# Kernel tuning notes

Measured on AMD Instinct MI355X. Metric: run time of the kernel, lower is better.

## Reference

```python
import jax, jax.numpy as jnp
import numpy as np

HIDDEN = 1024
NUM_HEADS = 16
HEAD_DIM = HIDDEN // NUM_HEADS


def rotary_cos_sin(seq_len, head_dim, dtype=jnp.float32):
    inv_freq = 1.0 / (10000.0 ** (jnp.arange(0, head_dim, 2, dtype=dtype) / head_dim))
    t = jnp.arange(seq_len, dtype=dtype)
    freqs = jnp.einsum('i,j->ij', t, inv_freq)          # [S, hd/2]
    emb = jnp.concatenate([freqs, freqs], axis=-1)      # [S, hd]
    return jnp.cos(emb), jnp.sin(emb)


def apply_rotary(x, cos, sin):
    # x: [B, H, S, hd]; cos/sin: [S, hd]
    x1, x2 = jnp.split(x, 2, axis=-1)
    x_rot = jnp.concatenate([-x2, x1], axis=-1)
    return x * cos + x_rot * sin


def setup_inputs() -> dict:
    key = jax.random.key(0)
    ks = jax.random.split(key, 5)
    S, B = 2048, 2
    x = jax.random.normal(ks[0], (S, B, HIDDEN), dtype=jnp.float32)
    s = 1.0 / np.sqrt(HIDDEN)
    W_qkv = jax.random.uniform(ks[1], (HIDDEN, 3 * HIDDEN), jnp.float32, -s, s)
    b_qkv = jax.random.uniform(ks[2], (3 * HIDDEN,), jnp.float32, -s, s)
    W_out = jax.random.uniform(ks[3], (HIDDEN, HIDDEN), jnp.float32, -s, s)
    b_out = jax.random.uniform(ks[4], (HIDDEN,), jnp.float32, -s, s)
    return {"x": x, "W_qkv": W_qkv, "b_qkv": b_qkv, "W_out": W_out, "b_out": b_out}


def reference(x, W_qkv, b_qkv, W_out, b_out):
    S, B, D = x.shape
    scale = HEAD_DIM ** -0.5
    qkv = x @ W_qkv + b_qkv                               # [S, B, 3D]
    qkv = qkv.reshape(S, B, NUM_HEADS, 3 * HEAD_DIM)
    q, k, v = jnp.split(qkv, 3, axis=-1)                  # each [S, B, H, hd]
    q = q.transpose(1, 2, 0, 3)                           # [B, H, S, hd]
    k = k.transpose(1, 2, 0, 3)
    v = v.transpose(1, 2, 0, 3)
    cos, sin = rotary_cos_sin(S, HEAD_DIM, x.dtype)
    q = apply_rotary(q, cos, sin)
    k = apply_rotary(k, cos, sin)
    scores = jnp.einsum('bhqd,bhkd->bhqk', q, k) * scale  # [B, H, S, S]
    weights = jax.nn.softmax(scores, axis=-1)
    attn = jnp.einsum('bhqk,bhkd->bhqd', weights, v)      # [B, H, S, hd]
    attn = attn.transpose(2, 0, 1, 3).reshape(S, B, D)    # [S, B, D]
    return attn @ W_out + b_out
```

## Files before the change

### kernel.cpp

```cpp
#include <hip/hip_runtime.h>

typedef unsigned short u16;
typedef __attribute__((ext_vector_type(8))) short bf16x8;
typedef __attribute__((ext_vector_type(4))) float f32x4;

#define S_LEN 2048
#define BATCH 2
#define HID 1024
#define NH 16
#define HD 64
#define MROWS 4096
#define QKV_N 3072
#define QSCALE 0.18033688011112042f

__device__ __forceinline__ u16 f2bf(float f) {
  unsigned u = __float_as_uint(f);
  u += 0x7fffu + ((u >> 16) & 1u);
  return (u16)(u >> 16);
}

__device__ __forceinline__ float bf2f(u16 u) {
  return __uint_as_float((unsigned)u << 16);
}

__device__ __forceinline__ float fexp2(float x) {
  float r; asm("v_exp_f32 %0, %1" : "=v"(r) : "v"(x)); return r;
}

__device__ __forceinline__ unsigned cvtpk(float lo, float hi) {
  unsigned r; asm("v_cvt_pk_bf16_f32 %0, %1, %2" : "=v"(r) : "v"(lo), "v"(hi)); return r;
}

__device__ __forceinline__ void gl2lds16(const u16* src, u16* lds) {
  __builtin_amdgcn_global_load_lds((__attribute__((address_space(1))) void*)(void*)src,
                                   (__attribute__((address_space(3))) void*)(void*)lds,
                                   16, 0, 0);
}

__device__ __forceinline__ void castT_body(const float* __restrict__ W, u16* __restrict__ Wt,
                                           int Ncols, int Krows, int bx, int by,
                                           float (*tile)[33]) {
  int c0 = bx * 32, r0 = by * 32;
  int tx = threadIdx.x & 31, ty = threadIdx.x >> 5;
  #pragma unroll
  for (int i = 0; i < 4; ++i)
    tile[ty + i * 8][tx] = W[(size_t)(r0 + ty + i * 8) * Ncols + c0 + tx];
  __syncthreads();
  #pragma unroll
  for (int i = 0; i < 4; ++i) {
    int a = ty + i * 8;
    Wt[(size_t)(c0 + a) * Krows + r0 + tx] = f2bf(tile[tx][a]);
  }
}

__global__ __launch_bounds__(256) void prep(
    const float* __restrict__ x, const float* __restrict__ W_qkv,
    const float* __restrict__ W_out, u16* __restrict__ xb,
    u16* __restrict__ Wqt, u16* __restrict__ Wot, float2* __restrict__ rope) {
  __shared__ float tile[32][33];
  const int bid = blockIdx.x;
  if (bid < 2048) {
    int i = bid * 256 + threadIdx.x;
    const float4* p = (const float4*)x;
    float4 a = p[2 * i], b = p[2 * i + 1];
    union { u16 us[8]; uint4 v; } o;
    o.us[0] = f2bf(a.x); o.us[1] = f2bf(a.y); o.us[2] = f2bf(a.z); o.us[3] = f2bf(a.w);
    o.us[4] = f2bf(b.x); o.us[5] = f2bf(b.y); o.us[6] = f2bf(b.z); o.us[7] = f2bf(b.w);
    *(uint4*)&xb[8 * i] = o.v;
  } else if (bid < 2048 + 3072) {
    int r = bid - 2048;
    castT_body(W_qkv, Wqt, QKV_N, HID, r % 96, r / 96, tile);
  } else if (bid < 2048 + 3072 + 1024) {
    int r = bid - (2048 + 3072);
    castT_body(W_out, Wot, HID, HID, r % 32, r / 32, tile);
  } else {
    int i = (bid - 6144) * 256 + threadIdx.x;
    int s = i >> 5, j = i & 31;
    float invf = powf(10000.0f, -(float)(2 * j) / 64.0f);
    float ang = (float)s * invf;
    rope[i] = make_float2(cosf(ang), sinf(ang));
  }
}

__global__ __launch_bounds__(256, 2) void gemm_qkv(
    const u16* __restrict__ A, const u16* __restrict__ Bt,
    const float* __restrict__ bias, const float2* __restrict__ rope,
    u16* __restrict__ Qb, u16* __restrict__ Kb, u16* __restrict__ Vb) {
  __shared__ u16 As[128 * 32];
  __shared__ u16 Bs[128 * 32];
  const int tid = threadIdx.x;
  const int lane = tid & 63, wid = tid >> 6;
  const int g = lane >> 4, l15 = lane & 15;
  const int bm0 = blockIdx.x * 128, bn0 = blockIdx.y * 128;
  const int wm = wid >> 1, wn = wid & 1;

  f32x4 acc[4][4] = {};
  for (int kt = 0; kt < 32; ++kt) {
    const int k0 = kt * 32;
    __syncthreads();
    #pragma unroll
    for (int it = 0; it < 2; ++it) {
      int s = it * 256 + tid;
      gl2lds16(A  + (size_t)(bm0 + (s >> 2)) * 1024 + k0 + (s & 3) * 8, &As[s * 8]);
      gl2lds16(Bt + (size_t)(bn0 + (s >> 2)) * 1024 + k0 + (s & 3) * 8, &Bs[s * 8]);
    }
    __syncthreads();
    bf16x8 af[4], bfr[4];
    #pragma unroll
    for (int m = 0; m < 4; ++m) af[m]  = *(const bf16x8*)&As[(wm * 64 + m * 16 + l15) * 32 + g * 8];
    #pragma unroll
    for (int n = 0; n < 4; ++n) bfr[n] = *(const bf16x8*)&Bs[(wn * 64 + n * 16 + l15) * 32 + g * 8];
    #pragma unroll
    for (int m = 0; m < 4; ++m)
      #pragma unroll
      for (int n = 0; n < 4; ++n)
        acc[m][n] = __builtin_amdgcn_mfma_f32_16x16x32_bf16(af[m], bfr[n], acc[m][n], 0, 0, 0);
  }

  const int cw0 = bn0 + wn * 64;
  const int gi = cw0 >> 6;
  const int h = gi / 3, tt = gi % 3;
  float bs[4];
  #pragma unroll
  for (int n = 0; n < 4; ++n) bs[n] = bias[cw0 + n * 16 + l15];
  const size_t hb = (size_t)h * (S_LEN * HD);

  if (tt == 2) {
    #pragma unroll
    for (int m = 0; m < 4; ++m)
      #pragma unroll
      for (int reg = 0; reg < 4; ++reg) {
        int r = bm0 + wm * 64 + m * 16 + g * 4 + reg;
        int srow = r >> 1, b = r & 1;
        size_t o = (size_t)(b * NH) * (S_LEN * HD) + hb + (size_t)srow * HD;
        #pragma unroll
        for (int n = 0; n < 4; ++n)
          Vb[o + n * 16 + l15] = f2bf(acc[m][n][reg] + bs[n]);
      }
  } else {
    u16* dst = (tt == 0) ? Qb : Kb;
    const float scl = (tt == 0) ? QSCALE : 1.0f;
    #pragma unroll
    for (int m = 0; m < 4; ++m)
      #pragma unroll
      for (int reg = 0; reg < 4; ++reg) {
        int r = bm0 + wm * 64 + m * 16 + g * 4 + reg;
        int srow = r >> 1, b = r & 1;
        size_t o = (size_t)(b * NH) * (S_LEN * HD) + hb + (size_t)srow * HD;
        #pragma unroll
        for (int n = 0; n < 2; ++n) {
          int dlo = n * 16 + l15;
          float2 cs = rope[srow * 32 + dlo];
          float v1 = acc[m][n][reg] + bs[n];
          float v2 = acc[m][n + 2][reg] + bs[n + 2];
          dst[o + dlo]      = f2bf((v1 * cs.x - v2 * cs.y) * scl);
          dst[o + dlo + 32] = f2bf((v2 * cs.x + v1 * cs.y) * scl);
        }
      }
  }
}

__global__ __launch_bounds__(256) void transpose_v(const u16* __restrict__ Vb, u16* __restrict__ Vt) {
  __shared__ u16 t[64][72];
  const int bh = blockIdx.y, s0 = blockIdx.x * 64;
  const size_t base = (size_t)bh * S_LEN * HD;
  const int tid = threadIdx.x;
  #pragma unroll
  for (int it = 0; it < 2; ++it) {
    int sl = it * 256 + tid;
    int r = sl >> 3, cg = sl & 7;
    union { uint4 v; u16 us[8]; } u;
    u.v = *(const uint4*)&Vb[base + (size_t)(s0 + r) * HD + cg * 8];
    #pragma unroll
    for (int j = 0; j < 8; ++j) t[cg * 8 + j][r] = u.us[j];
  }
  __syncthreads();
  #pragma unroll
  for (int it = 0; it < 2; ++it) {
    int sl = it * 256 + tid;
    int d = sl >> 3, sg = sl & 7;
    union { uint4 v; u16 us[8]; } u;
    #pragma unroll
    for (int j = 0; j < 8; ++j) u.us[j] = t[d][sg * 8 + j];
    *(uint4*)&Vt[(size_t)bh * HD * S_LEN + (size_t)d * S_LEN + s0 + sg * 8] = u.v;
  }
}

__global__ __launch_bounds__(512, 8) void attn_fwd(
    const u16* __restrict__ Qb, const u16* __restrict__ Kb,
    const u16* __restrict__ Vt, u16* __restrict__ part0,
    u16* __restrict__ part1, float2* __restrict__ stats) {
  __shared__ u16 Ks[2][64 * 64];
  __shared__ u16 Vs[2][64 * 64];
  const int tid = threadIdx.x;
  const int lane = tid & 63, wid = tid >> 6;
  const int g = lane >> 4, l15 = lane & 15;
  const int bh = blockIdx.y;
  const int split = blockIdx.z;
  const int kt0 = split * 16;
  const int qr0 = blockIdx.x * 128 + wid * 16;
  const u16* Qp = Qb + ((size_t)bh * S_LEN + qr0) * HD;
  const u16* Kp = Kb + (size_t)bh * S_LEN * HD;
  const u16* Vp = Vt + (size_t)bh * HD * S_LEN;

  const int sr = tid >> 3;
  const int ssw = (tid & 7) ^ (sr & 7);
  const u16* kg = Kp + (size_t)sr * HD + ssw * 8;
  const u16* vg = Vp + (size_t)sr * S_LEN + ssw * 8;

  bf16x8 qf[2];
  #pragma unroll
  for (int c = 0; c < 2; ++c) qf[c] = *(const bf16x8*)&Qp[l15 * HD + g * 8 + c * 32];

  f32x4 po[4] = {};
  float mrun = -INFINITY, lrun = 0.f;

  gl2lds16(kg + (size_t)kt0 * 64 * HD, &Ks[0][tid * 8]);
  gl2lds16(vg + kt0 * 64, &Vs[0][tid * 8]);
  __syncthreads();

  for (int i = 0; i < 16; ++i) {
    const int bb = i & 1;
    if (i + 1 < 16) {
      gl2lds16(kg + (size_t)(kt0 + i + 1) * 64 * HD, &Ks[bb ^ 1][tid * 8]);
      gl2lds16(vg + (kt0 + i + 1) * 64, &Vs[bb ^ 1][tid * 8]);
    }
    const u16* KsB = Ks[bb];
    const u16* VsB = Vs[bb];

    f32x4 sacc[4] = {};
    __builtin_amdgcn_s_setprio(1);
    #pragma unroll
    for (int c = 0; c < 2; ++c) {
      const int csw = ((g + 4 * c) ^ (l15 & 7)) * 8;
      #pragma unroll
      for (int t = 0; t < 4; ++t) {
        const bf16x8 kf = *(const bf16x8*)&KsB[(t * 16 + l15) * 64 + csw];
        sacc[t] = __builtin_amdgcn_mfma_f32_16x16x32_bf16(kf, qf[c], sacc[t], 0, 0, 0);
      }
    }
    __builtin_amdgcn_s_setprio(0);

    float m0 = fmaxf(fmaxf(sacc[0][0], sacc[0][1]), sacc[0][2]);
    float m1 = fmaxf(fmaxf(sacc[0][3], sacc[1][0]), sacc[1][1]);
    float m2 = fmaxf(fmaxf(sacc[1][2], sacc[1][3]), sacc[2][0]);
    float m3 = fmaxf(fmaxf(sacc[2][1], sacc[2][2]), sacc[2][3]);
    float m4 = fmaxf(fmaxf(sacc[3][0], sacc[3][1]), sacc[3][2]);
    float tm = fmaxf(fmaxf(fmaxf(m0, m1), fmaxf(m2, m3)), fmaxf(m4, sacc[3][3]));
    tm = fmaxf(tm, __shfl_xor(tm, 16));
    tm = fmaxf(tm, __shfl_xor(tm, 32));

    if (!__all(tm <= mrun + 8.f)) {
      float mnew = fmaxf(mrun, tm);
      float alpha = fexp2(mrun - mnew);
      mrun = mnew;
      lrun *= alpha;
      float ar[4];
      #pragma unroll
      for (int reg = 0; reg < 4; ++reg) ar[reg] = __shfl(alpha, g * 4 + reg);
      #pragma unroll
      for (int n = 0; n < 4; ++n)
        #pragma unroll
        for (int reg = 0; reg < 4; ++reg) po[n][reg] *= ar[reg];
    }

    unsigned u00, u01, u10, u11, u20, u21, u30, u31;
    float rsA, rsB;
    {
      float p0 = fexp2(sacc[0][0] - mrun), p1 = fexp2(sacc[0][1] - mrun);
      float p2 = fexp2(sacc[0][2] - mrun), p3 = fexp2(sacc[0][3] - mrun);
      u00 = cvtpk(p0, p1); u01 = cvtpk(p2, p3);
      rsA = (p0 + p1) + (p2 + p3);
      p0 = fexp2(sacc[1][0] - mrun); p1 = fexp2(sacc[1][1] - mrun);
      p2 = fexp2(sacc[1][2] - mrun); p3 = fexp2(sacc[1][3] - mrun);
      u10 = cvtpk(p0, p1); u11 = cvtpk(p2, p3);
      rsA += (p0 + p1) + (p2 + p3);
      p0 = fexp2(sacc[2][0] - mrun); p1 = fexp2(sacc[2][1] - mrun);
      p2 = fexp2(sacc[2][2] - mrun); p3 = fexp2(sacc[2][3] - mrun);
      u20 = cvtpk(p0, p1); u21 = cvtpk(p2, p3);
      rsB = (p0 + p1) + (p2 + p3);
      p0 = fexp2(sacc[3][0] - mrun); p1 = fexp2(sacc[3][1] - mrun);
      p2 = fexp2(sacc[3][2] - mrun); p3 = fexp2(sacc[3][3] - mrun);
      u30 = cvtpk(p0, p1); u31 = cvtpk(p2, p3);
      rsB += (p0 + p1) + (p2 + p3);
    }
    float rs = rsA + rsB;
    rs += __shfl_xor(rs, 16);
    rs += __shfl_xor(rs, 32);
    lrun += rs;

    asm("v_permlane32_swap_b32 %0, %1" : "+v"(u00), "+v"(u10));
    asm("v_permlane32_swap_b32 %0, %1" : "+v"(u01), "+v"(u11));
    asm("v_permlane32_swap_b32 %0, %1" : "+v"(u20), "+v"(u30));
    asm("v_permlane32_swap_b32 %0, %1" : "+v"(u21), "+v"(u31));
    asm("v_permlane16_swap_b32 %0, %1" : "+v"(u00), "+v"(u10));
    asm("v_permlane16_swap_b32 %0, %1" : "+v"(u01), "+v"(u11));
    asm("v_permlane16_swap_b32 %0, %1" : "+v"(u20), "+v"(u31 == u31 ? u30 : u30));
    asm("v_permlane16_swap_b32 %0, %1" : "+v"(u21), "+v"(u31));
    union { unsigned w[4]; bf16x8 v; } af0, af1;
    af0.w[0] = u00; af0.w[1] = u01; af0.w[2] = u10; af0.w[3] = u11;
    af1.w[0] = u20; af1.w[1] = u21; af1.w[2] = u30; af1.w[3] = u31;

    __builtin_amdgcn_s_setprio(1);
    #pragma unroll
    for (int c = 0; c < 2; ++c) {
      const bf16x8 pf = c ? af1.v : af0.v;
      const int csw = ((g + 4 * c) ^ (l15 & 7)) * 8;
      #pragma unroll
      for (int n = 0; n < 4; ++n) {
        const bf16x8 vf = *(const bf16x8*)&VsB[(n * 16 + l15) * 64 + csw];
        po[n] = __builtin_amdgcn_mfma_f32_16x16x32_bf16(pf, vf, po[n], 0, 0, 0);
      }
    }
    __builtin_amdgcn_s_setprio(0);
    __syncthreads();
  }

  u16* part = split ? part1 : part0;
  if (g == 0)
    stats[(size_t)split * (32 * 2048) + (size_t)bh * 2048 + qr0 + l15] =
        make_float2(mrun, lrun);
  #pragma unroll
  for (int n = 0; n < 4; ++n)
    #pragma unroll
    for (int reg = 0; reg < 4; ++reg) {
      size_t q = (size_t)bh * 2048 + qr0 + g * 4 + reg;
      part[q * 64 + n * 16 + l15] = f2bf(po[n][reg]);
    }
}

__global__ void attn_combine(const u16* __restrict__ part0, const u16* __restrict__ part1,
                             const float2* __restrict__ stats, u16* __restrict__ attn2d) {
  int t = blockIdx.x * 256 + threadIdx.x;
  int bh = t >> 14, r = t & 16383, q = r >> 3, dc = r & 7;
  int b = bh >> 4, h = bh & 15;
  float2 s0 = stats[bh * 2048 + q];
  float2 s1 = stats[32 * 2048 + bh * 2048 + q];
  float M = fmaxf(s0.x, s1.x);
  float w0 = fexp2(s0.x - M), w1 = fexp2(s1.x - M);
  float inv = 1.f / (w0 * s0.y + w1 * s1.y);
  w0 *= inv; w1 *= inv;
  size_t off = ((size_t)bh * 2048 + q) * 64 + dc * 8;
  union { uint4 v; u16 us[8]; } a, c, o;
  a.v = *(const uint4*)&part0[off];
  c.v = *(const uint4*)&part1[off];
  #pragma unroll
  for (int j = 0; j < 8; ++j)
    o.us[j] = f2bf(w0 * bf2f(a.us[j]) + w1 * bf2f(c.us[j]));
  *(uint4*)&attn2d[((size_t)q * BATCH + b) * HID + h * HD + dc * 8] = o.v;
}

__global__ __launch_bounds__(256, 2) void gemm_out(
    const u16* __restrict__ A, const u16* __restrict__ Bt,
    const float* __restrict__ bias, float* __restrict__ out) {
  __shared__ u16 As[128 * 32];
  __shared__ u16 Bs[64 * 32];
  const int tid = threadIdx.x;
  const int lane = tid & 63, wid = tid >> 6;
  const int g = lane >> 4, l15 = lane & 15;
  const int bm0 = blockIdx.x * 128, bn0 = blockIdx.y * 64;

  f32x4 acc[2][4] = {};
  for (int kt = 0; kt < 32; ++kt) {
    const int k0 = kt * 32;
    __syncthreads();
    #pragma unroll
    for (int it = 0; it < 2; ++it) {
      int s = it * 256 + tid;
      gl2lds16(A + (size_t)(bm0 + (s >> 2)) * 1024 + k0 + (s & 3) * 8, &As[s * 8]);
    }
    gl2lds16(Bt + (size_t)(bn0 + (tid >> 2)) * 1024 + k0 + (tid & 3) * 8, &Bs[tid * 8]);
    __syncthreads();
    bf16x8 af[2], bfr[4];
    #pragma unroll
    for (int m = 0; m < 2; ++m) af[m]  = *(const bf16x8*)&As[(wid * 32 + m * 16 + l15) * 32 + g * 8];
    #pragma unroll
    for (int n = 0; n < 4; ++n) bfr[n] = *(const bf16x8*)&Bs[(n * 16 + l15) * 32 + g * 8];
    #pragma unroll
    for (int m = 0; m < 2; ++m)
      #pragma unroll
      for (int n = 0; n < 4; ++n)
        acc[m][n] = __builtin_amdgcn_mfma_f32_16x16x32_bf16(af[m], bfr[n], acc[m][n], 0, 0, 0);
  }
  #pragma unroll
  for (int n = 0; n < 4; ++n) {
    int c = bn0 + n * 16 + l15;
    float bv = bias[c];
    #pragma unroll
    for (int m = 0; m < 2; ++m)
      #pragma unroll
      for (int reg = 0; reg < 4; ++reg) {
        int r = bm0 + wid * 32 + m * 16 + g * 4 + reg;
        out[(size_t)r * HID + c] = acc[m][n][reg] + bv;
      }
  }
}

extern "C" void kernel_launch(void* const* d_in, const int* in_sizes, int n_in,
                              void* d_out, int out_size, void* d_ws, size_t ws_size,
                              hipStream_t stream) {
  const float* x     = (const float*)d_in[0];
  const float* W_qkv = (const float*)d_in[1];
  const float* b_qkv = (const float*)d_in[2];
  const float* W_out = (const float*)d_in[3];
  const float* b_out = (const float*)d_in[4];
  float* out = (float*)d_out;

  char* ws = (char*)d_ws;
  size_t off = 0;
  auto carve = [&](size_t bytes) { void* p = ws + off; off += (bytes + 255) & ~(size_t)255; return p; };
  u16* xb      = (u16*)carve((size_t)MROWS * HID * 2);
  u16* Wqt     = (u16*)carve((size_t)QKV_N * HID * 2);
  u16* Wot     = (u16*)carve((size_t)HID * HID * 2);
  float2* rope = (float2*)carve((size_t)S_LEN * 32 * 8);
  u16* Qb      = (u16*)carve((size_t)BATCH * NH * S_LEN * HD * 2);
  u16* Kb      = (u16*)carve((size_t)BATCH * NH * S_LEN * HD * 2);
  u16* Vb      = (u16*)carve((size_t)BATCH * NH * S_LEN * HD * 2);
  u16* Vt      = (u16*)carve((size_t)BATCH * NH * S_LEN * HD * 2);
  u16* attn2d  = (u16*)carve((size_t)MROWS * HID * 2);
  float2* stats= (float2*)carve((size_t)2 * 32 * 2048 * 8);

  prep<<<6400, 256, 0, stream>>>(x, W_qkv, W_out, xb, Wqt, Wot, rope);
  gemm_qkv<<<dim3(MROWS / 128, QKV_N / 128), 256, 0, stream>>>(xb, Wqt, b_qkv, rope, Qb, Kb, Vb);
  transpose_v<<<dim3(S_LEN / 64, BATCH * NH), 256, 0, stream>>>(Vb, Vt);
  attn_fwd<<<dim3(S_LEN / 128, BATCH * NH, 2), 512, 0, stream>>>(Qb, Kb, Vt, xb, Vb, stats);
  attn_combine<<<2048, 256, 0, stream>>>(xb, Vb, stats, attn2d);
  gemm_out<<<dim3(MROWS / 128, HID / 64), 256, 0, stream>>>(attn2d, Wot, b_out, out);
}
```

Before: 132.6 us.

## Switch attention to 32x32x16 MFMA tiles with 32 query rows per wave

Rewrites the attention forward kernel to use 32x32x16 bf16 MFMA instructions, so each wave handles 32 query rows instead of 16. This halves the number of blocks, and the K rows are permuted at load time so the P fragments line up with the MFMA input layout without permlane swaps. It also remaps the grid to 1D so the two splits of the same head are adjacent, lowers the occupancy hint, and replaces powf with exp2 in the rope table. The larger accumulators raise register pressure, and the halved block count may leave the GPU under-occupied.

```diff
diff --git a/kernel.cpp b/kernel.cpp
--- a/kernel.cpp
+++ b/kernel.cpp
@@ -3,6 +3,7 @@
 typedef unsigned short u16;
 typedef __attribute__((ext_vector_type(8))) short bf16x8;
 typedef __attribute__((ext_vector_type(4))) float f32x4;
+typedef __attribute__((ext_vector_type(16))) float f32x16;
 
 #define S_LEN 2048
 #define BATCH 2
@@ -76,7 +77,7 @@
   } else {
     int i = (bid - 6144) * 256 + threadIdx.x;
     int s = i >> 5, j = i & 31;
-    float invf = powf(10000.0f, -(float)(2 * j) / 64.0f);
+    float invf = fexp2(-(float)(2 * j) * (13.287712379549449f / 64.0f));
     float ang = (float)s * invf;
     rope[i] = make_float2(cosf(ang), sinf(ang));
   }
@@ -186,7 +187,7 @@
   }
 }
 
-__global__ __launch_bounds__(512, 8) void attn_fwd(
+__global__ __launch_bounds__(512, 4) void attn_fwd(
     const u16* __restrict__ Qb, const u16* __restrict__ Kb,
     const u16* __restrict__ Vt, u16* __restrict__ part0,
     u16* __restrict__ part1, float2* __restrict__ stats) {
@@ -194,25 +195,28 @@
   __shared__ u16 Vs[2][64 * 64];
   const int tid = threadIdx.x;
   const int lane = tid & 63, wid = tid >> 6;
-  const int g = lane >> 4, l15 = lane & 15;
-  const int bh = blockIdx.y;
-  const int split = blockIdx.z;
+  const int l31 = lane & 31, h = lane >> 5;
+  const int pp = blockIdx.x & 63;
+  const int bh = pp >> 1, split = pp & 1;
   const int kt0 = split * 16;
-  const int qr0 = blockIdx.x * 128 + wid * 16;
-  const u16* Qp = Qb + ((size_t)bh * S_LEN + qr0) * HD;
+  const int qw0 = (blockIdx.x >> 6) * 256 + wid * 32;
+  const u16* Qp = Qb + ((size_t)bh * S_LEN + qw0) * HD;
   const u16* Kp = Kb + (size_t)bh * S_LEN * HD;
   const u16* Vp = Vt + (size_t)bh * HD * S_LEN;
 
-  const int sr = tid >> 3;
-  const int ssw = (tid & 7) ^ (sr & 7);
-  const u16* kg = Kp + (size_t)sr * HD + ssw * 8;
+  const int sr = tid >> 3, tc = tid & 7;
+  const int ssw = tc ^ (sr & 7);
+  const int act = ((sr >> 4) & 1) * 16 + ((sr >> 2) & 1) * 8
+                + ((sr & 3) | (((sr >> 3) & 1) << 2)) + (sr >> 5) * 32;
+  const u16* kg = Kp + (size_t)act * HD + ssw * 8;
   const u16* vg = Vp + (size_t)sr * S_LEN + ssw * 8;
 
-  bf16x8 qf[2];
-  #pragma unroll
-  for (int c = 0; c < 2; ++c) qf[c] = *(const bf16x8*)&Qp[l15 * HD + g * 8 + c * 32];
-
-  f32x4 po[4] = {};
+  bf16x8 qf0 = *(const bf16x8*)&Qp[(size_t)l31 * HD +  0 + h * 8];
+  bf16x8 qf1 = *(const bf16x8*)&Qp[(size_t)l31 * HD + 16 + h * 8];
+  bf16x8 qf2 = *(const bf16x8*)&Qp[(size_t)l31 * HD + 32 + h * 8];
+  bf16x8 qf3 = *(const bf16x8*)&Qp[(size_t)l31 * HD + 48 + h * 8];
+
+  f32x16 po0 = {}, po1 = {};
   float mrun = -INFINITY, lrun = 0.f;
 
   gl2lds16(kg + (size_t)kt0 * 64 * HD, &Ks[0][tid * 8]);
@@ -228,26 +232,22 @@
     const u16* KsB = Ks[bb];
     const u16* VsB = Vs[bb];
 
-    f32x4 sacc[4] = {};
+    f32x16 s0 = {}, s1 = {};
     __builtin_amdgcn_s_setprio(1);
     #pragma unroll
-    for (int c = 0; c < 2; ++c) {
-      const int csw = ((g + 4 * c) ^ (l15 & 7)) * 8;
-      #pragma unroll
-      for (int t = 0; t < 4; ++t) {
-        const bf16x8 kf = *(const bf16x8*)&KsB[(t * 16 + l15) * 64 + csw];
-        sacc[t] = __builtin_amdgcn_mfma_f32_16x16x32_bf16(kf, qf[c], sacc[t], 0, 0, 0);
-      }
+    for (int s = 0; s < 4; ++s) {
+      const bf16x8 qf = (s == 0) ? qf0 : (s == 1) ? qf1 : (s == 2) ? qf2 : qf3;
+      const int csw = ((2 * s + h) ^ (l31 & 7)) * 8;
+      bf16x8 kf0 = *(const bf16x8*)&KsB[l31 * 64 + csw];
+      s0 = __builtin_amdgcn_mfma_f32_32x32x16_bf16(kf0, qf, s0, 0, 0, 0);
+      bf16x8 kf1 = *(const bf16x8*)&KsB[(32 + l31) * 64 + csw];
+      s1 = __builtin_amdgcn_mfma_f32_32x32x16_bf16(kf1, qf, s1, 0, 0, 0);
     }
     __builtin_amdgcn_s_setprio(0);
 
-    float m0 = fmaxf(fmaxf(sacc[0][0], sacc[0][1]), sacc[0][2]);
-    float m1 = fmaxf(fmaxf(sacc[0][3], sacc[1][0]), sacc[1][1]);
-    float m2 = fmaxf(fmaxf(sacc[1][2], sacc[1][3]), sacc[2][0]);
-    float m3 = fmaxf(fmaxf(sacc[2][1], sacc[2][2]), sacc[2][3]);
-    float m4 = fmaxf(fmaxf(sacc[3][0], sacc[3][1]), sacc[3][2]);
-    float tm = fmaxf(fmaxf(fmaxf(m0, m1), fmaxf(m2, m3)), fmaxf(m4, sacc[3][3]));
-    tm = fmaxf(tm, __shfl_xor(tm, 16));
+    float tm = -INFINITY;
+    #pragma unroll
+    for (int r = 0; r < 16; ++r) tm = fmaxf(tm, fmaxf(s0[r], s1[r]));
     tm = fmaxf(tm, __shfl_xor(tm, 32));
 
     if (!__all(tm <= mrun + 8.f)) {
@@ -255,78 +255,60 @@
       float alpha = fexp2(mrun - mnew);
       mrun = mnew;
       lrun *= alpha;
-      float ar[4];
-      #pragma unroll
-      for (int reg = 0; reg < 4; ++reg) ar[reg] = __shfl(alpha, g * 4 + reg);
-      #pragma unroll
-      for (int n = 0; n < 4; ++n)
-        #pragma unroll
-        for (int reg = 0; reg < 4; ++reg) po[n][reg] *= ar[reg];
-    }
-
-    unsigned u00, u01, u10, u11, u20, u21, u30, u31;
-    float rsA, rsB;
-    {
-      float p0 = fexp2(sacc[0][0] - mrun), p1 = fexp2(sacc[0][1] - mrun);
-      float p2 = fexp2(sacc[0][2] - mrun), p3 = fexp2(sacc[0][3] - mrun);
-      u00 = cvtpk(p0, p1); u01 = cvtpk(p2, p3);
-      rsA = (p0 + p1) + (p2 + p3);
-      p0 = fexp2(sacc[1][0] - mrun); p1 = fexp2(sacc[1][1] - mrun);
-      p2 = fexp2(sacc[1][2] - mrun); p3 = fexp2(sacc[1][3] - mrun);
-      u10 = cvtpk(p0, p1); u11 = cvtpk(p2, p3);
-      rsA += (p0 + p1) + (p2 + p3);
-      p0 = fexp2(sacc[2][0] - mrun); p1 = fexp2(sacc[2][1] - mrun);
-      p2 = fexp2(sacc[2][2] - mrun); p3 = fexp2(sacc[2][3] - mrun);
-      u20 = cvtpk(p0, p1); u21 = cvtpk(p2, p3);
-      rsB = (p0 + p1) + (p2 + p3);
-      p0 = fexp2(sacc[3][0] - mrun); p1 = fexp2(sacc[3][1] - mrun);
-      p2 = fexp2(sacc[3][2] - mrun); p3 = fexp2(sacc[3][3] - mrun);
-      u30 = cvtpk(p0, p1); u31 = cvtpk(p2, p3);
-      rsB += (p0 + p1) + (p2 + p3);
-    }
-    float rs = rsA + rsB;
-    rs += __shfl_xor(rs, 16);
+      #pragma unroll
+      for (int r = 0; r < 16; ++r) {
+        float ar = __shfl(alpha, (r & 3) + 8 * (r >> 2) + 4 * h);
+        po0[r] *= ar;
+        po1[r] *= ar;
+      }
+    }
+
+    float rs = 0.f;
+    unsigned pwa[8], pwb[8];
+    #pragma unroll
+    for (int w = 0; w < 8; ++w) {
+      float a = fexp2(s0[2 * w] - mrun), b = fexp2(s0[2 * w + 1] - mrun);
+      rs += a + b;
+      pwa[w] = cvtpk(a, b);
+    }
+    #pragma unroll
+    for (int w = 0; w < 8; ++w) {
+      float a = fexp2(s1[2 * w] - mrun), b = fexp2(s1[2 * w + 1] - mrun);
+      rs += a + b;
+      pwb[w] = cvtpk(a, b);
+    }
     rs += __shfl_xor(rs, 32);
     lrun += rs;
 
-    asm("v_permlane32_swap_b32 %0, %1" : "+v"(u00), "+v"(u10));
-    asm("v_permlane32_swap_b32 %0, %1" : "+v"(u01), "+v"(u11));
-    asm("v_permlane32_swap_b32 %0, %1" : "+v"(u20), "+v"(u30));
-    asm("v_permlane32_swap_b32 %0, %1" : "+v"(u21), "+v"(u31));
-    asm("v_permlane16_swap_b32 %0, %1" : "+v"(u00), "+v"(u10));
-    asm("v_permlane16_swap_b32 %0, %1" : "+v"(u01), "+v"(u11));
-    asm("v_permlane16_swap_b32 %0, %1" : "+v"(u20), "+v"(u31 == u31 ? u30 : u30));
-    asm("v_permlane16_swap_b32 %0, %1" : "+v"(u21), "+v"(u31));
-    union { unsigned w[4]; bf16x8 v; } af0, af1;
-    af0.w[0] = u00; af0.w[1] = u01; af0.w[2] = u10; af0.w[3] = u11;
-    af1.w[0] = u20; af1.w[1] = u21; af1.w[2] = u30; af1.w[3] = u31;
-
     __builtin_amdgcn_s_setprio(1);
     #pragma unroll
-    for (int c = 0; c < 2; ++c) {
-      const bf16x8 pf = c ? af1.v : af0.v;
-      const int csw = ((g + 4 * c) ^ (l15 & 7)) * 8;
-      #pragma unroll
-      for (int n = 0; n < 4; ++n) {
-        const bf16x8 vf = *(const bf16x8*)&VsB[(n * 16 + l15) * 64 + csw];
-        po[n] = __builtin_amdgcn_mfma_f32_16x16x32_bf16(pf, vf, po[n], 0, 0, 0);
-      }
+    for (int s = 0; s < 4; ++s) {
+      union { unsigned w[4]; bf16x8 v; } pf;
+      if (s == 0)      { pf.w[0] = pwa[0]; pf.w[1] = pwa[1]; pf.w[2] = pwa[2]; pf.w[3] = pwa[3]; }
+      else if (s == 1) { pf.w[0] = pwa[4]; pf.w[1] = pwa[5]; pf.w[2] = pwa[6]; pf.w[3] = pwa[7]; }
+      else if (s == 2) { pf.w[0] = pwb[0]; pf.w[1] = pwb[1]; pf.w[2] = pwb[2]; pf.w[3] = pwb[3]; }
+      else             { pf.w[0] = pwb[4]; pf.w[1] = pwb[5]; pf.w[2] = pwb[6]; pf.w[3] = pwb[7]; }
+      const int csw = ((2 * s + h) ^ (l31 & 7)) * 8;
+      bf16x8 vf0 = *(const bf16x8*)&VsB[l31 * 64 + csw];
+      po0 = __builtin_amdgcn_mfma_f32_32x32x16_bf16(pf.v, vf0, po0, 0, 0, 0);
+      bf16x8 vf1 = *(const bf16x8*)&VsB[(32 + l31) * 64 + csw];
+      po1 = __builtin_amdgcn_mfma_f32_32x32x16_bf16(pf.v, vf1, po1, 0, 0, 0);
     }
     __builtin_amdgcn_s_setprio(0);
     __syncthreads();
   }
 
   u16* part = split ? part1 : part0;
-  if (g == 0)
-    stats[(size_t)split * (32 * 2048) + (size_t)bh * 2048 + qr0 + l15] =
+  if (h == 0)
+    stats[(size_t)split * (32 * 2048) + (size_t)bh * 2048 + qw0 + l31] =
         make_float2(mrun, lrun);
   #pragma unroll
-  for (int n = 0; n < 4; ++n)
-    #pragma unroll
-    for (int reg = 0; reg < 4; ++reg) {
-      size_t q = (size_t)bh * 2048 + qr0 + g * 4 + reg;
-      part[q * 64 + n * 16 + l15] = f2bf(po[n][reg]);
-    }
+  for (int r = 0; r < 16; ++r) {
+    int q = qw0 + (r & 3) + 8 * (r >> 2) + 4 * h;
+    size_t o = ((size_t)bh * 2048 + q) * 64 + l31;
+    part[o]      = f2bf(po0[r]);
+    part[o + 32] = f2bf(po1[r]);
+  }
 }
 
 __global__ void attn_combine(const u16* __restrict__ part0, const u16* __restrict__ part1,
@@ -423,7 +405,7 @@
   prep<<<6400, 256, 0, stream>>>(x, W_qkv, W_out, xb, Wqt, Wot, rope);
   gemm_qkv<<<dim3(MROWS / 128, QKV_N / 128), 256, 0, stream>>>(xb, Wqt, b_qkv, rope, Qb, Kb, Vb);
   transpose_v<<<dim3(S_LEN / 64, BATCH * NH), 256, 0, stream>>>(Vb, Vt);
-  attn_fwd<<<dim3(S_LEN / 128, BATCH * NH, 2), 512, 0, stream>>>(Qb, Kb, Vt, xb, Vb, stats);
+  attn_fwd<<<512, 512, 0, stream>>>(Qb, Kb, Vt, xb, Vb, stats);
   attn_combine<<<2048, 256, 0, stream>>>(xb, Vb, stats, attn2d);
   gemm_out<<<dim3(MROWS / 128, HID / 64), 256, 0, stream>>>(attn2d, Wot, b_out, out);
 }
```

Result: faster. 124.5 us (-6.2%).
